# Performance work log

Measured on AMD Instinct MI355X. Metric: run time of the kernel, lower is better.

The kernel has to match this reference:

```python
import math
import jax, jax.numpy as jnp
import numpy as np

FACIL_RATE = 2.0
FIRE_THRESH = 0.85
MAX_GATE = 8.0
EPS = 1e-12  # F.normalize eps

B, T, D = 8, 4096, 2048


def _gelu(x):
    # tanh-approx GELU, exactly as in the torch module
    c = math.sqrt(2.0 / math.pi)
    return 0.5 * x * (1.0 + jnp.tanh(c * (x + 0.044715 * x * x * x)))


def _l2norm(v, axis=-1):
    n = jnp.sqrt(jnp.sum(v * v, axis=axis, keepdims=True))
    return v / jnp.maximum(n, EPS)


def setup_inputs() -> dict:
    key = jax.random.key(0)
    k1, k2 = jax.random.split(key)
    x = jax.random.normal(k1, (B, T, D), dtype=jnp.float32)
    pos_buf = jax.random.normal(k2, (T, D), dtype=jnp.float32)
    pos_facil = jnp.ones((T,), dtype=jnp.float32)
    log_k_pos = jnp.asarray(math.log(0.5), dtype=jnp.float32)
    return {"x": x, "log_k_pos": log_k_pos, "pos_buf": pos_buf, "pos_facil": pos_facil}


def reference(x, log_k_pos, pos_buf, pos_facil):
    # steady-state (pass1 complete) path of GELU275.forward
    k_pos = jnp.clip(jnp.exp(log_k_pos), 0.01, 5.0)
    y = _gelu(x)                                   # [B,T,D]
    # everything below the gelu except the final gate multiply runs under
    # no_grad / on y.detach() in torch -> stop_gradient here
    y_det = jax.lax.stop_gradient(y)
    pos_buf_n = _l2norm(jax.lax.stop_gradient(pos_buf))          # [T,D]
    y_n = _l2norm(y_det)                                          # [B,T,D]
    sim = jnp.einsum("btd,td->bt", y_n, pos_buf_n)               # cosine sim [B,T]
    fire_mask = jnp.mean(sim, axis=0) > FIRE_THRESH              # [T]
    pf = jax.lax.stop_gradient(pos_facil)
    facil_t = jnp.where(fire_mask, jnp.minimum(pf * FACIL_RATE, 16.0), pf)  # [T]
    gate = jnp.minimum(1.0 + k_pos * (facil_t[None, :] - 1.0) * sim, MAX_GATE)  # [B,T]
    return y * gate[:, :, None]
```

## Files before the change

kernel.cpp:

```cpp
#include <hip/hip_runtime.h>
#include <math.h>

#define BB 8
#define TT 4096
#define DD 2048
#define THREADS 512
#define CHUNKS 8

typedef float v4f __attribute__((ext_vector_type(4)));

__device__ __forceinline__ float fast_tanh(float a) {
    float e = __expf(2.0f * a);
    return 1.0f - 2.0f / (e + 1.0f);
}

__device__ __forceinline__ float gelu_tanh(float x) {
    const float c = 0.7978845608028654f;
    float inner = c * (x + 0.044715f * x * x * x);
    return 0.5f * x * (1.0f + fast_tanh(inner));
}

__global__ __launch_bounds__(THREADS) void gelu275_fused(
    const float* __restrict__ x,
    const float* __restrict__ log_k_pos,
    const float* __restrict__ pos_buf,
    const float* __restrict__ pos_facil,
    float* __restrict__ out)
{
    const int t    = blockIdx.x;
    const int tid  = threadIdx.x;
    const int lane = tid & 63;
    const int wave = tid >> 6;

    __shared__ float s_dot[BB];
    __shared__ float s_yn2[BB];
    __shared__ float s_pn2;

    const float* xrow = x       + ((size_t)wave * TT + t) * DD;
    const float* prow = pos_buf + (size_t)t * DD;
    const int    base = lane * 4;

    v4f xv[CHUNKS], pv[CHUNKS];
#pragma unroll
    for (int c = 0; c < CHUNKS; ++c)
        xv[c] = *reinterpret_cast<const v4f*>(xrow + c * 256 + base);
#pragma unroll
    for (int c = 0; c < CHUNKS; ++c)
        pv[c] = *reinterpret_cast<const v4f*>(prow + c * 256 + base);

    float dot = 0.0f, yn2 = 0.0f, pn2 = 0.0f;
#pragma unroll
    for (int c = 0; c < CHUNKS; ++c) {
        v4f& v = xv[c];
        const v4f& p = pv[c];
        v.x = gelu_tanh(v.x); v.y = gelu_tanh(v.y);
        v.z = gelu_tanh(v.z); v.w = gelu_tanh(v.w);
        dot += v.x * p.x + v.y * p.y + v.z * p.z + v.w * p.w;
        yn2 += v.x * v.x + v.y * v.y + v.z * v.z + v.w * v.w;
        pn2 += p.x * p.x + p.y * p.y + p.z * p.z + p.w * p.w;
    }

#pragma unroll
    for (int off = 32; off; off >>= 1) {
        dot += __shfl_xor(dot, off);
        yn2 += __shfl_xor(yn2, off);
        pn2 += __shfl_xor(pn2, off);
    }
    if (lane == 0) {
        s_dot[wave] = dot;
        s_yn2[wave] = yn2;
        if (wave == 0) s_pn2 = pn2;
    }
    __syncthreads();

    const float kp = fminf(fmaxf(__expf(log_k_pos[0]), 0.01f), 5.0f);
    const float pn = fmaxf(sqrtf(s_pn2), 1e-12f);

    float simsum = 0.0f;
    float simw   = 0.0f;
#pragma unroll
    for (int b = 0; b < BB; ++b) {
        const float s = s_dot[b] / (fmaxf(sqrtf(s_yn2[b]), 1e-12f) * pn);
        simsum += s;
        if (b == wave) simw = s;
    }
    const bool  fire  = (simsum * (1.0f / BB)) > 0.85f;
    const float pf    = pos_facil[t];
    const float facil = fire ? fminf(pf * 2.0f, 16.0f) : pf;
    const float g     = fminf(1.0f + kp * (facil - 1.0f) * simw, 8.0f);

    float* orow = out + ((size_t)wave * TT + t) * DD;
#pragma unroll
    for (int c = 0; c < CHUNKS; ++c) {
        v4f o;
        o.x = xv[c].x * g; o.y = xv[c].y * g;
        o.z = xv[c].z * g; o.w = xv[c].w * g;
        *reinterpret_cast<v4f*>(orow + c * 256 + base) = o;
    }
}

extern "C" void kernel_launch(void* const* d_in, const int* in_sizes, int n_in,
                              void* d_out, int out_size, void* d_ws, size_t ws_size,
                              hipStream_t stream) {
    const float* x          = (const float*)d_in[0];
    const float* log_k_pos  = (const float*)d_in[1];
    const float* pos_buf    = (const float*)d_in[2];
    const float* pos_facil  = (const float*)d_in[3];
    float* out              = (float*)d_out;

    dim3 grid(TT);
    dim3 block(THREADS);
    gelu275_fused<<<grid, block, 0, stream>>>(x, log_k_pos, pos_buf, pos_facil, out);
}
```

Measured before the change: 126.6 us.

## Recompute GELU from reloaded x instead of holding row in registers

The kernel no longer keeps the x and pos_buf chunks in registers across the block reduction. It reloads x in the output loop and recomputes GELU there. GELU becomes a sigmoid-form expression using one exp and a hardware reciprocal, the similarity division uses rcp, and launch bounds request higher occupancy. The aim is lower register pressure and more waves in flight to hide memory latency, at the cost of a second read of x (possibly hitting cache) and duplicated GELU math.

New measurement: 134.4 us. +6.2%, slower.

```diff
diff --git a/kernel.cpp b/kernel.cpp
--- a/kernel.cpp
+++ b/kernel.cpp
@@ -9,18 +9,16 @@
 
 typedef float v4f __attribute__((ext_vector_type(4)));
 
-__device__ __forceinline__ float fast_tanh(float a) {
-    float e = __expf(2.0f * a);
-    return 1.0f - 2.0f / (e + 1.0f);
+__device__ __forceinline__ float gelu_fast(float x) {
+    const float c1 = 1.5957691216057308f;
+    const float c2 = 0.07135481282556483f;
+    float x2 = x * x;
+    float tt = fmaf(c2, x2, c1);
+    float e  = __expf(-x * tt);
+    return x * __builtin_amdgcn_rcpf(1.0f + e);
 }
 
-__device__ __forceinline__ float gelu_tanh(float x) {
-    const float c = 0.7978845608028654f;
-    float inner = c * (x + 0.044715f * x * x * x);
-    return 0.5f * x * (1.0f + fast_tanh(inner));
-}
-
-__global__ __launch_bounds__(THREADS) void gelu275_fused(
+__global__ __launch_bounds__(THREADS, 8) void gelu275_fused(
     const float* __restrict__ x,
     const float* __restrict__ log_k_pos,
     const float* __restrict__ pos_buf,
@@ -40,24 +38,18 @@
     const float* prow = pos_buf + (size_t)t * DD;
     const int    base = lane * 4;
 
-    v4f xv[CHUNKS], pv[CHUNKS];
-#pragma unroll
-    for (int c = 0; c < CHUNKS; ++c)
-        xv[c] = *reinterpret_cast<const v4f*>(xrow + c * 256 + base);
-#pragma unroll
-    for (int c = 0; c < CHUNKS; ++c)
-        pv[c] = *reinterpret_cast<const v4f*>(prow + c * 256 + base);
-
     float dot = 0.0f, yn2 = 0.0f, pn2 = 0.0f;
 #pragma unroll
     for (int c = 0; c < CHUNKS; ++c) {
-        v4f& v = xv[c];
-        const v4f& p = pv[c];
-        v.x = gelu_tanh(v.x); v.y = gelu_tanh(v.y);
-        v.z = gelu_tanh(v.z); v.w = gelu_tanh(v.w);
-        dot += v.x * p.x + v.y * p.y + v.z * p.z + v.w * p.w;
-        yn2 += v.x * v.x + v.y * v.y + v.z * v.z + v.w * v.w;
-        pn2 += p.x * p.x + p.y * p.y + p.z * p.z + p.w * p.w;
+        const v4f xv = *reinterpret_cast<const v4f*>(xrow + c * 256 + base);
+        const v4f pv = *reinterpret_cast<const v4f*>(prow + c * 256 + base);
+        const float y0 = gelu_fast(xv.x);
+        const float y1 = gelu_fast(xv.y);
+        const float y2 = gelu_fast(xv.z);
+        const float y3 = gelu_fast(xv.w);
+        dot += y0 * pv.x + y1 * pv.y + y2 * pv.z + y3 * pv.w;
+        yn2 += y0 * y0 + y1 * y1 + y2 * y2 + y3 * y3;
+        pn2 += pv.x * pv.x + pv.y * pv.y + pv.z * pv.z + pv.w * pv.w;
     }
 
 #pragma unroll
@@ -80,7 +72,8 @@
     float simw   = 0.0f;
 #pragma unroll
     for (int b = 0; b < BB; ++b) {
-        const float s = s_dot[b] / (fmaxf(sqrtf(s_yn2[b]), 1e-12f) * pn);
+        const float s = s_dot[b] *
+            __builtin_amdgcn_rcpf(fmaxf(sqrtf(s_yn2[b]), 1e-12f) * pn);
         simsum += s;
         if (b == wave) simw = s;
     }
@@ -92,9 +85,12 @@
     float* orow = out + ((size_t)wave * TT + t) * DD;
 #pragma unroll
     for (int c = 0; c < CHUNKS; ++c) {
+        const v4f xv = *reinterpret_cast<const v4f*>(xrow + c * 256 + base);
         v4f o;
-        o.x = xv[c].x * g; o.y = xv[c].y * g;
-        o.z = xv[c].z * g; o.w = xv[c].w * g;
+        o.x = gelu_fast(xv.x) * g;
+        o.y = gelu_fast(xv.y) * g;
+        o.z = gelu_fast(xv.z) * g;
+        o.w = gelu_fast(xv.w) * g;
         *reinterpret_cast<v4f*>(orow + c * 256 + base) = o;
     }
 }
```

## Process multiple timesteps per block with register double-buffered prefetch and cheaper GELU

Applied to the files above, without the earlier changes.

Each block now handles 8 consecutive timesteps instead of one. It prefetches the next timestep's x row and pos_buf row into a second register buffer while the current one is computed, and alternates two shared reduction slots separated by raw barriers. GELU is rewritten as x*sigmoid form with a hardware reciprocal, and the division in the cosine is replaced by rcp. The aim is to hide load latency and cut per-block launch and sync overhead on a memory-bound kernel, at the cost of higher register pressure (now with a launch-bounds occupancy hint) and fewer blocks.

Measured after the change: 124.2 us. About the same (-1.9%).

```diff
diff --git a/kernel.cpp b/kernel.cpp
--- a/kernel.cpp
+++ b/kernel.cpp
@@ -5,59 +5,50 @@
 #define TT 4096
 #define DD 2048
 #define THREADS 512
-#define CHUNKS 8
+#define NT 8
+#define NBLK (TT / NT)
 
 typedef float v4f __attribute__((ext_vector_type(4)));
 
-__device__ __forceinline__ float fast_tanh(float a) {
-    float e = __expf(2.0f * a);
-    return 1.0f - 2.0f / (e + 1.0f);
+__device__ __forceinline__ float gelu_fast(float x) {
+    const float c1 = 1.5957691216057308f;
+    const float c2 = 0.07135481282556483f;
+    float e = __expf(-x * fmaf(c2, x * x, c1));
+    return x * __builtin_amdgcn_rcpf(1.0f + e);
 }
 
-__device__ __forceinline__ float gelu_tanh(float x) {
-    const float c = 0.7978845608028654f;
-    float inner = c * (x + 0.044715f * x * x * x);
-    return 0.5f * x * (1.0f + fast_tanh(inner));
-}
+__device__ __forceinline__ void do_step(
+    const float* __restrict__ x, const float* __restrict__ pos_buf,
+    const float* __restrict__ pos_facil, float* __restrict__ out,
+    int t, int par, bool last, int lane, int wave, float kp,
+    v4f (&CUR)[8], v4f (&NXT)[8], v4f (&P)[8],
+    float (&s_red)[2][17])
+{
+    const int base = lane * 4;
 
-__global__ __launch_bounds__(THREADS) void gelu275_fused(
-    const float* __restrict__ x,
-    const float* __restrict__ log_k_pos,
-    const float* __restrict__ pos_buf,
-    const float* __restrict__ pos_facil,
-    float* __restrict__ out)
-{
-    const int t    = blockIdx.x;
-    const int tid  = threadIdx.x;
-    const int lane = tid & 63;
-    const int wave = tid >> 6;
+    if (!last) {
+        const float* xr = x + ((size_t)wave * TT + (t + 1)) * DD + base;
+#pragma unroll
+        for (int c = 0; c < 8; ++c) NXT[c] = *(const v4f*)(xr + c * 256);
+    }
 
-    __shared__ float s_dot[BB];
-    __shared__ float s_yn2[BB];
-    __shared__ float s_pn2;
-
-    const float* xrow = x       + ((size_t)wave * TT + t) * DD;
-    const float* prow = pos_buf + (size_t)t * DD;
-    const int    base = lane * 4;
-
-    v4f xv[CHUNKS], pv[CHUNKS];
+    float dot = 0.f, yn2 = 0.f, pn2 = 0.f;
 #pragma unroll
-    for (int c = 0; c < CHUNKS; ++c)
-        xv[c] = *reinterpret_cast<const v4f*>(xrow + c * 256 + base);
-#pragma unroll
-    for (int c = 0; c < CHUNKS; ++c)
-        pv[c] = *reinterpret_cast<const v4f*>(prow + c * 256 + base);
-
-    float dot = 0.0f, yn2 = 0.0f, pn2 = 0.0f;
-#pragma unroll
-    for (int c = 0; c < CHUNKS; ++c) {
-        v4f& v = xv[c];
-        const v4f& p = pv[c];
-        v.x = gelu_tanh(v.x); v.y = gelu_tanh(v.y);
-        v.z = gelu_tanh(v.z); v.w = gelu_tanh(v.w);
+    for (int c = 0; c < 8; ++c) {
+        v4f v = CUR[c];
+        v.x = gelu_fast(v.x); v.y = gelu_fast(v.y);
+        v.z = gelu_fast(v.z); v.w = gelu_fast(v.w);
+        CUR[c] = v;
+        const v4f p = P[c];
         dot += v.x * p.x + v.y * p.y + v.z * p.z + v.w * p.w;
         yn2 += v.x * v.x + v.y * v.y + v.z * v.z + v.w * v.w;
         pn2 += p.x * p.x + p.y * p.y + p.z * p.z + p.w * p.w;
+    }
+
+    if (!last) {
+        const float* pr = pos_buf + (size_t)(t + 1) * DD + base;
+#pragma unroll
+        for (int c = 0; c < 8; ++c) P[c] = *(const v4f*)(pr + c * 256);
     }
 
 #pragma unroll
@@ -67,35 +58,71 @@
         pn2 += __shfl_xor(pn2, off);
     }
     if (lane == 0) {
-        s_dot[wave] = dot;
-        s_yn2[wave] = yn2;
-        if (wave == 0) s_pn2 = pn2;
+        s_red[par][wave]      = dot;
+        s_red[par][BB + wave] = yn2;
+        if (wave == 0) s_red[par][16] = pn2;
     }
-    __syncthreads();
+    asm volatile("s_waitcnt lgkmcnt(0)" ::: "memory");
+    __builtin_amdgcn_s_barrier();
+    asm volatile("" ::: "memory");
 
-    const float kp = fminf(fmaxf(__expf(log_k_pos[0]), 0.01f), 5.0f);
-    const float pn = fmaxf(sqrtf(s_pn2), 1e-12f);
-
-    float simsum = 0.0f;
-    float simw   = 0.0f;
+    const float pnn = fmaxf(sqrtf(s_red[par][16]), 1e-12f);
+    float simsum = 0.f, simw = 0.f;
 #pragma unroll
     for (int b = 0; b < BB; ++b) {
-        const float s = s_dot[b] / (fmaxf(sqrtf(s_yn2[b]), 1e-12f) * pn);
+        const float s = s_red[par][b] *
+            __builtin_amdgcn_rcpf(fmaxf(sqrtf(s_red[par][BB + b]), 1e-12f) * pnn);
         simsum += s;
         if (b == wave) simw = s;
     }
-    const bool  fire  = (simsum * (1.0f / BB)) > 0.85f;
+    const bool  fire  = (simsum * 0.125f) > 0.85f;
     const float pf    = pos_facil[t];
     const float facil = fire ? fminf(pf * 2.0f, 16.0f) : pf;
     const float g     = fminf(1.0f + kp * (facil - 1.0f) * simw, 8.0f);
 
-    float* orow = out + ((size_t)wave * TT + t) * DD;
+    float* orow = out + ((size_t)wave * TT + t) * DD + base;
 #pragma unroll
-    for (int c = 0; c < CHUNKS; ++c) {
-        v4f o;
-        o.x = xv[c].x * g; o.y = xv[c].y * g;
-        o.z = xv[c].z * g; o.w = xv[c].w * g;
-        *reinterpret_cast<v4f*>(orow + c * 256 + base) = o;
+    for (int c = 0; c < 8; ++c) {
+        v4f o = CUR[c];
+        o.x *= g; o.y *= g; o.z *= g; o.w *= g;
+        *(v4f*)(orow + c * 256) = o;
+    }
+}
+
+__global__ __launch_bounds__(THREADS, 4) void gelu275_fused(
+    const float* __restrict__ x,
+    const float* __restrict__ log_k_pos,
+    const float* __restrict__ pos_buf,
+    const float* __restrict__ pos_facil,
+    float* __restrict__ out)
+{
+    const int tid  = threadIdx.x;
+    const int lane = tid & 63;
+    const int wave = tid >> 6;
+    const int t0   = blockIdx.x * NT;
+
+    __shared__ float s_red[2][17];
+
+    const float kp  = fminf(fmaxf(__expf(log_k_pos[0]), 0.01f), 5.0f);
+    const int  base = lane * 4;
+
+    v4f A[8], B[8], P[8];
+
+    {
+        const float* xr = x + ((size_t)wave * TT + t0) * DD + base;
+#pragma unroll
+        for (int c = 0; c < 8; ++c) A[c] = *(const v4f*)(xr + c * 256);
+        const float* pr = pos_buf + (size_t)t0 * DD + base;
+#pragma unroll
+        for (int c = 0; c < 8; ++c) P[c] = *(const v4f*)(pr + c * 256);
+    }
+
+#pragma unroll
+    for (int i = 0; i < NT; i += 2) {
+        do_step(x, pos_buf, pos_facil, out, t0 + i,     0, false,
+                lane, wave, kp, A, B, P, s_red);
+        do_step(x, pos_buf, pos_facil, out, t0 + i + 1, 1, (i + 2 >= NT),
+                lane, wave, kp, B, A, P, s_red);
     }
 }
 
@@ -108,7 +135,7 @@
     const float* pos_facil  = (const float*)d_in[3];
     float* out              = (float*)d_out;
 
-    dim3 grid(TT);
+    dim3 grid(NBLK);
     dim3 block(THREADS);
     gelu275_fused<<<grid, block, 0, stream>>>(x, log_k_pos, pos_buf, pos_facil, out);
 }
```
